# Performance work log

Measured on AMD Instinct MI355X. Metric: run time of the kernel, lower is better.

Reference implementation:

```python
import jax, jax.numpy as jnp
import numpy as np

P0, P1, P2 = 0, 9, 95          # player, status
P3 = 103                        # player_info end / cards start
P4 = P3 + 13 * 740              # 9723, cards end / potions start
P5 = P4 + 43                    # 9766, relics start
P6 = P5 + 180                   # 9946, monsters start
P7 = P6 + 5 * 101               # 10451


def setup_inputs() -> dict:
    key = jax.random.key(0)
    ks = jax.random.split(key, 8)
    def lin(k, out_f, in_f):
        # torch.nn.Linear default init: U(-1/sqrt(in), 1/sqrt(in)), weight [out, in]
        bound = 1.0 / np.sqrt(in_f)
        return jax.random.uniform(k, (out_f, in_f), jnp.float32, -bound, bound)
    return {
        "battle": jax.random.normal(ks[0], (32768, P7), jnp.float32),
        "W_player": lin(ks[1], 4, 9),
        "W_status": lin(ks[2], 16, 86),
        "W_pinfo": lin(ks[3], 2, 8),
        "W_card": lin(ks[4], 32, 740),
        "W_potions": lin(ks[5], 8, 43),
        "W_relics": lin(ks[6], 16, 180),
        "W_monster": lin(ks[7], 16, 101),
    }


def reference(battle, W_player, W_status, W_pinfo, W_card, W_potions, W_relics, W_monster):
    B = battle.shape[0]
    player = battle[:, P0:P1] @ W_player.T                     # [B, 4]
    status = battle[:, P1:P2] @ W_status.T                     # [B, 16]
    pinfo = battle[:, P2:P3] @ W_pinfo.T                       # [B, 2]
    # 13 card segments share one weight -> single batched GEMM
    cards = battle[:, P3:P4].reshape(B, 13, 740)
    cards = jnp.einsum('bsf,of->bso', cards, W_card).reshape(B, 13 * 32)
    potions = battle[:, P4:P5] @ W_potions.T                   # [B, 8]
    relics = battle[:, P5:P6] @ W_relics.T                     # [B, 16]
    # 5 monster segments share one weight
    monsters = battle[:, P6:P7].reshape(B, 5, 101)
    monsters = jnp.einsum('bsf,of->bso', monsters, W_monster).reshape(B, 5 * 16)
    # concat in the module's ModuleList order
    return jnp.concatenate([player, status, pinfo, cards, potions, relics, monsters], axis=-1)
```

## Files before the change

### kernel.cpp

```cpp
#include <hip/hip_runtime.h>
#include <stdint.h>


typedef __attribute__((ext_vector_type(8))) short short8;
typedef __attribute__((ext_vector_type(4))) float f32x4;

#define TOTAL_ELS (32768u * 10451u)

__device__ inline unsigned short f2bf(float f) {
  union { float f; uint32_t u; } v; v.f = f;
  uint32_t r = v.u + 0x7FFFu + ((v.u >> 16) & 1u);
  return (unsigned short)(r >> 16);
}

__device__ inline void gload_dw(const float* g, float* lds) {
  __builtin_amdgcn_global_load_lds(
      (const __attribute__((address_space(1))) void*)g,
      (__attribute__((address_space(3))) void*)lds, 4, 0, 0);
}

__global__ __launch_bounds__(256) void pack_w(const float* __restrict__ Wc,
                                              uint32_t* __restrict__ wout) {
  int el = blockIdx.x * 256 + threadIdx.x;
  if (el >= 12288) return;
  int d  = el & 3;
  int rl = (el >> 2) & 15;
  int kg = (el >> 6) & 3;
  int wn = (el >> 8) & 1;
  int cs = el >> 9;
  int s  = cs & 3, ch = cs >> 2;
  int n  = wn * 16 + rl;
  int k  = ch * 128 + s * 32 + kg * 8 + d * 2;
  float v0 = (k     < 740) ? Wc[n * 740 + k]     : 0.0f;
  float v1 = (k + 1 < 740) ? Wc[n * 740 + k + 1] : 0.0f;
  wout[el] = (uint32_t)f2bf(v0) | ((uint32_t)f2bf(v1) << 16);
}

__global__ __launch_bounds__(256, 2) void seg_gemm(
    const float* __restrict__ battle,
    const float* __restrict__ Wplayer, const float* __restrict__ Wstatus,
    const float* __restrict__ Wpinfo,  const float* __restrict__ Wpotions,
    const float* __restrict__ Wrelics, const float* __restrict__ Wmonster,
    const uint32_t* __restrict__ wpack2,
    float* __restrict__ out, const float* __restrict__ zpage)
{
  __shared__ float shm[19456];
  const int bid = blockIdx.x;
  const int t    = threadIdx.x;
  const int lane = t & 63;
  const int wv   = t >> 6;
  const int rl   = lane & 15;
  const int kg   = lane >> 4;

  if (bid < 16384) {
    const uint32_t g0 = (uint32_t)(bid * 2) * 10451u + 103u;
    const uint32_t g1 = g0 + 10451u;
    #pragma unroll
    for (int r = 0; r < 38; ++r)
      gload_dw(battle + g0 + (uint32_t)(r * 256 + t), &shm[r * 256 + t]);
    #pragma unroll
    for (int r = 0; r < 38; ++r)
      gload_dw(battle + g1 + (uint32_t)(r * 256 + t), &shm[9728 + r * 256 + t]);
    __syncthreads();

    const int wm = wv >> 1;
    const int wn = wv & 1;
    const float* aspan = &shm[wm * 9728];
    const uint32_t abase = (rl < 13) ? (uint32_t)(rl * 740) : 0u;

    f32x4 acc = {0.f, 0.f, 0.f, 0.f};
    for (int ch = 0; ch < 6; ++ch) {
      #pragma unroll
      for (int s = 0; s < 4; ++s) {
        const float* ap = aspan + abase + (uint32_t)(ch * 128 + s * 32 + kg * 8);
        f32x4 lo = *(const f32x4*)ap;
        f32x4 hi = *(const f32x4*)(ap + 4);
        short8 aa;
        aa[0] = (short)f2bf(lo[0]); aa[1] = (short)f2bf(lo[1]);
        aa[2] = (short)f2bf(lo[2]); aa[3] = (short)f2bf(lo[3]);
        aa[4] = (short)f2bf(hi[0]); aa[5] = (short)f2bf(hi[1]);
        aa[6] = (short)f2bf(hi[2]); aa[7] = (short)f2bf(hi[3]);
        const int cs = ch * 4 + s;
        short8 wf = *(const short8*)(wpack2 + (uint32_t)(cs * 512 + wn * 256 + kg * 64 + rl * 4));
        acc = __builtin_amdgcn_mfma_f32_16x16x32_bf16(aa, wf, acc, 0, 0, 0);
      }
    }

    const uint32_t b = (uint32_t)(bid * 2 + wm);
    #pragma unroll
    for (int q = 0; q < 4; ++q) {
      const int sub = kg * 4 + q;
      if (sub < 13)
        out[b * 542u + 22u + (uint32_t)(sub * 32 + wn * 16 + rl)] = acc[q];
    }
    return;
  }

  const int sb = bid - 16384;
  int bloc, nsub, K, NOUT, soff, ooff;
  const float* wp;
  if (sb < 1280)      { bloc = sb;        nsub = 5; K = 101; NOUT = 16; soff = 9946; ooff = 462; wp = Wmonster; }
  else if (sb < 1536) { bloc = sb - 1280; nsub = 1; K = 180; NOUT = 16; soff = 9766; ooff = 446; wp = Wrelics; }
  else if (sb < 1792) { bloc = sb - 1536; nsub = 1; K = 86;  NOUT = 16; soff = 9;    ooff = 4;   wp = Wstatus; }
  else if (sb < 2048) { bloc = sb - 1792; nsub = 1; K = 43;  NOUT = 8;  soff = 9723; ooff = 438; wp = Wpotions; }
  else if (sb < 2304) { bloc = sb - 2048; nsub = 1; K = 9;   NOUT = 4;  soff = 0;    ooff = 0;   wp = Wplayer; }
  else                { bloc = sb - 2304; nsub = 1; K = 8;   NOUT = 2;  soff = 95;   ooff = 20;  wp = Wpinfo; }

  float* lds_a = shm;
  float* lds_w = shm + 4096;

  const int mb = bloc * 128;
  const int r0 = t >> 5;

  uint32_t rb[16];
  #pragma unroll
  for (int i = 0; i < 16; ++i) {
    uint32_t m   = (uint32_t)(mb + r0 + 8 * i);
    uint32_t b   = m / (uint32_t)nsub;
    uint32_t sub = m - b * (uint32_t)nsub;
    rb[i] = b * 10451u + (uint32_t)soff + sub * (uint32_t)K;
  }

  const int klin = t & 31;
  const int lk   = (((klin >> 2) ^ r0) << 2) | (klin & 3);

  f32x4 acc[2] = {};
  const int nch = (K + 31) >> 5;

  for (int ch = 0; ch < nch; ++ch) {
    const int kk = (ch << 5) + lk;
    #pragma unroll
    for (int i = 0; i < 16; ++i) {
      const float* sp = (kk < K) ? (battle + rb[i] + kk) : zpage;
      gload_dw(sp, &lds_a[i * 256 + t]);
    }
    #pragma unroll
    for (int i = 0; i < 4; ++i) {
      const int col = r0 + 8 * i;
      const float* sp = (col < NOUT && kk < K) ? (wp + col * K + kk) : zpage;
      gload_dw(sp, &lds_w[i * 256 + t]);
    }
    __syncthreads();

    short8 af[2], bfr;
    #pragma unroll
    for (int mf = 0; mf < 2; ++mf) {
      const int r  = wv * 32 + mf * 16 + rl;
      const int g0i = (2 * kg) ^ (r & 7);
      const int g1i = (2 * kg + 1) ^ (r & 7);
      f32x4 lo = *(const f32x4*)&lds_a[r * 32 + g0i * 4];
      f32x4 hi = *(const f32x4*)&lds_a[r * 32 + g1i * 4];
      af[mf][0] = (short)f2bf(lo[0]); af[mf][1] = (short)f2bf(lo[1]);
      af[mf][2] = (short)f2bf(lo[2]); af[mf][3] = (short)f2bf(lo[3]);
      af[mf][4] = (short)f2bf(hi[0]); af[mf][5] = (short)f2bf(hi[1]);
      af[mf][6] = (short)f2bf(hi[2]); af[mf][7] = (short)f2bf(hi[3]);
    }
    {
      const int c   = rl;
      const int g0i = (2 * kg) ^ (c & 7);
      const int g1i = (2 * kg + 1) ^ (c & 7);
      f32x4 lo = *(const f32x4*)&lds_w[c * 32 + g0i * 4];
      f32x4 hi = *(const f32x4*)&lds_w[c * 32 + g1i * 4];
      bfr[0] = (short)f2bf(lo[0]); bfr[1] = (short)f2bf(lo[1]);
      bfr[2] = (short)f2bf(lo[2]); bfr[3] = (short)f2bf(lo[3]);
      bfr[4] = (short)f2bf(hi[0]); bfr[5] = (short)f2bf(hi[1]);
      bfr[6] = (short)f2bf(hi[2]); bfr[7] = (short)f2bf(hi[3]);
    }
    #pragma unroll
    for (int mf = 0; mf < 2; ++mf)
      acc[mf] = __builtin_amdgcn_mfma_f32_16x16x32_bf16(af[mf], bfr, acc[mf], 0, 0, 0);

    __syncthreads();
  }

  #pragma unroll
  for (int mf = 0; mf < 2; ++mf) {
    #pragma unroll
    for (int q = 0; q < 4; ++q) {
      uint32_t m   = (uint32_t)(mb + wv * 32 + mf * 16 + kg * 4 + q);
      uint32_t b   = m / (uint32_t)nsub;
      uint32_t sub = m - b * (uint32_t)nsub;
      uint32_t ob  = b * 542u + (uint32_t)ooff + sub * (uint32_t)NOUT;
      const int col = rl;
      if (col < NOUT) out[ob + col] = acc[mf][q];
    }
  }
}

extern "C" void kernel_launch(void* const* d_in, const int* in_sizes, int n_in,
                              void* d_out, int out_size, void* d_ws, size_t ws_size,
                              hipStream_t stream) {
  const float* battle   = (const float*)d_in[0];
  const float* Wplayer  = (const float*)d_in[1];
  const float* Wstatus  = (const float*)d_in[2];
  const float* Wpinfo   = (const float*)d_in[3];
  const float* Wcard    = (const float*)d_in[4];
  const float* Wpotions = (const float*)d_in[5];
  const float* Wrelics  = (const float*)d_in[6];
  const float* Wmonster = (const float*)d_in[7];
  float* out = (float*)d_out;

  const float* zpage = (const float*)d_ws;
  uint32_t* wpack2 = (uint32_t*)((char*)d_ws + 256);

  hipMemsetAsync(d_ws, 0, 256, stream);
  hipLaunchKernelGGL(pack_w, dim3(48), dim3(256), 0, stream, Wcard, wpack2);
  hipLaunchKernelGGL(seg_gemm, dim3(18944), dim3(256), 0, stream,
                     battle, Wplayer, Wstatus, Wpinfo, Wpotions, Wrelics,
                     Wmonster, (const uint32_t*)wpack2, out, zpage);
}
```

Before: 309.2 us.

## Make card blocks persistent over 16 rows with double-buffered LDS staging

Each card block now processes 16 batch rows instead of 2. It double-buffers the row staging in LDS so the next row's global-to-LDS loads overlap the current row's MFMA work, using explicit vmcnt waits and barriers. The K dimension is split across wave pairs, with an LDS reduction to combine them. Card blocks are interleaved with the small-segment blocks in a 5:4 pattern, so the grid shrinks from 18944 to 4608 blocks. The goal is to hide load latency and cut per-block launch overhead, at the cost of less parallelism per row, an extra barrier and reduction per row, and larger LDS use.

```diff
diff --git a/kernel.cpp b/kernel.cpp
--- a/kernel.cpp
+++ b/kernel.cpp
@@ -4,8 +4,6 @@
 
 typedef __attribute__((ext_vector_type(8))) short short8;
 typedef __attribute__((ext_vector_type(4))) float f32x4;
-
-#define TOTAL_ELS (32768u * 10451u)
 
 __device__ inline unsigned short f2bf(float f) {
   union { float f; uint32_t u; } v; v.f = f;
@@ -28,9 +26,8 @@
   int kg = (el >> 6) & 3;
   int wn = (el >> 8) & 1;
   int cs = el >> 9;
-  int s  = cs & 3, ch = cs >> 2;
   int n  = wn * 16 + rl;
-  int k  = ch * 128 + s * 32 + kg * 8 + d * 2;
+  int k  = cs * 32 + kg * 8 + d * 2;
   float v0 = (k     < 740) ? Wc[n * 740 + k]     : 0.0f;
   float v1 = (k + 1 < 740) ? Wc[n * 740 + k + 1] : 0.0f;
   wout[el] = (uint32_t)f2bf(v0) | ((uint32_t)f2bf(v1) << 16);
@@ -44,35 +41,49 @@
     const uint32_t* __restrict__ wpack2,
     float* __restrict__ out, const float* __restrict__ zpage)
 {
-  __shared__ float shm[19456];
-  const int bid = blockIdx.x;
+  __shared__ float shm[19968];
+  const int bid  = blockIdx.x;
   const int t    = threadIdx.x;
   const int lane = t & 63;
   const int wv   = t >> 6;
   const int rl   = lane & 15;
   const int kg   = lane >> 4;
 
-  if (bid < 16384) {
-    const uint32_t g0 = (uint32_t)(bid * 2) * 10451u + 103u;
-    const uint32_t g1 = g0 + 10451u;
-    #pragma unroll
-    for (int r = 0; r < 38; ++r)
-      gload_dw(battle + g0 + (uint32_t)(r * 256 + t), &shm[r * 256 + t]);
-    #pragma unroll
-    for (int r = 0; r < 38; ++r)
-      gload_dw(battle + g1 + (uint32_t)(r * 256 + t), &shm[9728 + r * 256 + t]);
-    __syncthreads();
-
-    const int wm = wv >> 1;
-    const int wn = wv & 1;
-    const float* aspan = &shm[wm * 9728];
+  const int g9 = bid / 9, r9 = bid - g9 * 9;
+
+  if (r9 >= 5) {
+    const int cb   = g9 * 4 + (r9 - 5);
+    const int row0 = cb * 16;
+    const int wn   = wv & 1;
+    const int wk   = wv >> 1;
     const uint32_t abase = (rl < 13) ? (uint32_t)(rl * 740) : 0u;
-
-    f32x4 acc = {0.f, 0.f, 0.f, 0.f};
-    for (int ch = 0; ch < 6; ++ch) {
+    float* wred = &shm[19456];
+
+    auto stagec = [&](int r, int pb) {
+      const uint32_t g = (uint32_t)(row0 + r) * 10451u + 103u;
+      float* dst = &shm[pb * 9728];
       #pragma unroll
-      for (int s = 0; s < 4; ++s) {
-        const float* ap = aspan + abase + (uint32_t)(ch * 128 + s * 32 + kg * 8);
+      for (int i = 0; i < 38; ++i)
+        gload_dw(battle + g + (uint32_t)(i * 256 + t), &dst[i * 256 + t]);
+    };
+
+    stagec(0, 0);
+
+    for (int r = 0; r < 16; ++r) {
+      if (r + 1 < 16) {
+        stagec(r + 1, (r + 1) & 1);
+        asm volatile("s_waitcnt vmcnt(38)" ::: "memory");
+      } else {
+        asm volatile("s_waitcnt vmcnt(0)" ::: "memory");
+      }
+      asm volatile("s_barrier" ::: "memory");
+
+      const float* abuf = &shm[(r & 1) * 9728];
+      f32x4 acc = {0.f, 0.f, 0.f, 0.f};
+      #pragma unroll
+      for (int si = 0; si < 12; ++si) {
+        const int cs = wk * 12 + si;
+        const float* ap = abuf + abase + (uint32_t)(cs * 32 + kg * 8);
         f32x4 lo = *(const f32x4*)ap;
         f32x4 hi = *(const f32x4*)(ap + 4);
         short8 aa;
@@ -80,23 +91,31 @@
         aa[2] = (short)f2bf(lo[2]); aa[3] = (short)f2bf(lo[3]);
         aa[4] = (short)f2bf(hi[0]); aa[5] = (short)f2bf(hi[1]);
         aa[6] = (short)f2bf(hi[2]); aa[7] = (short)f2bf(hi[3]);
-        const int cs = ch * 4 + s;
         short8 wf = *(const short8*)(wpack2 + (uint32_t)(cs * 512 + wn * 256 + kg * 64 + rl * 4));
         acc = __builtin_amdgcn_mfma_f32_16x16x32_bf16(aa, wf, acc, 0, 0, 0);
       }
-    }
-
-    const uint32_t b = (uint32_t)(bid * 2 + wm);
-    #pragma unroll
-    for (int q = 0; q < 4; ++q) {
-      const int sub = kg * 4 + q;
-      if (sub < 13)
-        out[b * 542u + 22u + (uint32_t)(sub * 32 + wn * 16 + rl)] = acc[q];
+
+      if (wk == 1) {
+        #pragma unroll
+        for (int q = 0; q < 4; ++q)
+          wred[wn * 256 + (kg * 4 + q) * 16 + rl] = acc[q];
+      }
+      asm volatile("s_barrier" ::: "memory");
+      if (wk == 0) {
+        const uint32_t ob = (uint32_t)(row0 + r) * 542u + 22u;
+        #pragma unroll
+        for (int q = 0; q < 4; ++q) {
+          const int sub = kg * 4 + q;
+          float v = acc[q] + wred[wn * 256 + (kg * 4 + q) * 16 + rl];
+          if (sub < 13)
+            out[ob + (uint32_t)(sub * 32 + wn * 16 + rl)] = v;
+        }
+      }
     }
     return;
   }
 
-  const int sb = bid - 16384;
+  const int sb = g9 * 5 + r9;
   int bloc, nsub, K, NOUT, soff, ooff;
   const float* wp;
   if (sb < 1280)      { bloc = sb;        nsub = 5; K = 101; NOUT = 16; soff = 9946; ooff = 462; wp = Wmonster; }
@@ -145,11 +164,11 @@
     short8 af[2], bfr;
     #pragma unroll
     for (int mf = 0; mf < 2; ++mf) {
-      const int r  = wv * 32 + mf * 16 + rl;
-      const int g0i = (2 * kg) ^ (r & 7);
-      const int g1i = (2 * kg + 1) ^ (r & 7);
-      f32x4 lo = *(const f32x4*)&lds_a[r * 32 + g0i * 4];
-      f32x4 hi = *(const f32x4*)&lds_a[r * 32 + g1i * 4];
+      const int rr  = wv * 32 + mf * 16 + rl;
+      const int g0i = (2 * kg) ^ (rr & 7);
+      const int g1i = (2 * kg + 1) ^ (rr & 7);
+      f32x4 lo = *(const f32x4*)&lds_a[rr * 32 + g0i * 4];
+      f32x4 hi = *(const f32x4*)&lds_a[rr * 32 + g1i * 4];
       af[mf][0] = (short)f2bf(lo[0]); af[mf][1] = (short)f2bf(lo[1]);
       af[mf][2] = (short)f2bf(lo[2]); af[mf][3] = (short)f2bf(lo[3]);
       af[mf][4] = (short)f2bf(hi[0]); af[mf][5] = (short)f2bf(hi[1]);
@@ -205,7 +224,7 @@
 
   hipMemsetAsync(d_ws, 0, 256, stream);
   hipLaunchKernelGGL(pack_w, dim3(48), dim3(256), 0, stream, Wcard, wpack2);
-  hipLaunchKernelGGL(seg_gemm, dim3(18944), dim3(256), 0, stream,
+  hipLaunchKernelGGL(seg_gemm, dim3(4608), dim3(256), 0, stream,
                      battle, Wplayer, Wstatus, Wpinfo, Wpotions, Wrelics,
                      Wmonster, (const uint32_t*)wpack2, out, zpage);
 }
```

After: 362.1 us. 17.1% more time.
